# Optimization experiments

Hardware: AMD Instinct MI355X
Metric: run time of the kernel (lower is better)

The kernel has to match this reference:

```python
import jax, jax.numpy as jnp
import numpy as np

SEQ = 2048
HID = 1024
NH = 16
HD = HID // NH


def setup_inputs() -> dict:
    key = jax.random.key(0)
    ks = jax.random.split(key, 5)
    s = 0.02
    return {
        "hidden_states": jax.random.normal(ks[0], (SEQ, HID), dtype=jnp.float32),
        "w_attn": jax.random.normal(ks[1], (HID, 3 * HID), dtype=jnp.float32) * s,
        "b_attn": jax.random.normal(ks[2], (3 * HID,), dtype=jnp.float32) * s,
        "w_proj": jax.random.normal(ks[3], (HID, HID), dtype=jnp.float32) * s,
        "b_proj": jax.random.normal(ks[4], (HID,), dtype=jnp.float32) * s,
    }


def reference(hidden_states, w_attn, b_attn, w_proj, b_proj):
    S = hidden_states.shape[0]
    qkv = hidden_states @ w_attn + b_attn          # [S, 3H]
    q, k, v = jnp.split(qkv, 3, axis=-1)
    q = q.reshape(S, NH, HD)
    k = k.reshape(S, NH, HD)
    v = v.reshape(S, NH, HD)
    sm_scale = 1.0 / np.sqrt(HD).astype(np.float32)
    # explicit scores [h, q, k] in fp32, as in the torch module
    scores = jnp.einsum('qhd,khd->hqk', q.astype(jnp.float32), k.astype(jnp.float32))
    scores = scores * sm_scale
    causal = jnp.tril(jnp.ones((S, S), dtype=bool))  # [q, k]
    scores = jnp.where(causal[None, :, :], scores, -jnp.inf)
    probs = jax.nn.softmax(scores, axis=-1)
    attn = jnp.einsum('hqk,khd->qhd', probs, v.astype(jnp.float32))  # [S, NH, HD]
    attn = attn.reshape(S, HID).astype(hidden_states.dtype)
    return attn @ w_proj + b_proj
```

## Files before the change

kernel.cpp:

```cpp
#include <hip/hip_runtime.h>
#include <cstdint>
#include <cstddef>

#define SEQ 2048
#define HID 1024
#define NHEAD 16
#define HDIM 64

typedef _Float16 f16;
typedef f16 half8 __attribute__((ext_vector_type(8)));
typedef f16 half4 __attribute__((ext_vector_type(4)));
typedef f16 half2_ __attribute__((ext_vector_type(2)));
typedef float f32x4 __attribute__((ext_vector_type(4)));

#define ASYNC_COPY16(g, l)                                                    \
  __builtin_amdgcn_global_load_lds(                                           \
      (const __attribute__((address_space(1))) void*)(const void*)(g),        \
      (__attribute__((address_space(3))) void*)(void*)(l), 16, 0, 0)

__global__ __launch_bounds__(256) void prologue(
    const float* __restrict__ h, const float* __restrict__ wa,
    const float* __restrict__ wp, f16* __restrict__ h16,
    f16* __restrict__ waT, f16* __restrict__ wpT) {
  const int b = blockIdx.x, tid = threadIdx.x;
  if (b >= 1024) {
    int i = ((b - 1024) * 256 + tid) * 8;
    float4 v0 = *(const float4*)(h + i);
    float4 v1 = *(const float4*)(h + i + 4);
    half8 o;
    o[0] = (f16)v0.x; o[1] = (f16)v0.y; o[2] = (f16)v0.z; o[3] = (f16)v0.w;
    o[4] = (f16)v1.x; o[5] = (f16)v1.y; o[6] = (f16)v1.z; o[7] = (f16)v1.w;
    *(half8*)(h16 + i) = o;
    return;
  }
  const float* src; f16* dst; int C, bx, by;
  if (b < 768) { src = wa; dst = waT; C = 3072; bx = b % 48; by = b / 48; }
  else { int t = b - 768; src = wp; dst = wpT; C = 1024; bx = t & 15; by = t >> 4; }
  __shared__ float tile[64][65];
  const int tx = tid & 63, ty = tid >> 6;
  const int c0 = bx * 64, r0 = by * 64;
#pragma unroll
  for (int i = 0; i < 64; i += 4)
    tile[ty + i][tx] = src[(size_t)(r0 + ty + i) * C + c0 + tx];
  __syncthreads();
#pragma unroll
  for (int i = 0; i < 64; i += 4)
    dst[(size_t)(c0 + ty + i) * 1024 + r0 + tx] = (f16)tile[tx][ty + i];
}

template <int BM, int BN, bool OUT16>
__global__ __launch_bounds__(256) void gemm_f16(
    const f16* __restrict__ A, const f16* __restrict__ Bt,
    const float* __restrict__ bias, void* __restrict__ Cout, int M, int N,
    int K) {
  constexpr int FM = BM / 32, FN = BN / 32;
  __shared__ __align__(16) f16 sA[BM * 64];
  __shared__ __align__(16) f16 sB[BN * 64];
  const int tid = threadIdx.x;
  const int wave = tid >> 6, lane = tid & 63;
  const int quad = lane >> 4, l16 = lane & 15;
  const int m0 = blockIdx.y * BM, n0 = blockIdx.x * BN;
  const int wm = (wave >> 1) * (BM / 2), wn = (wave & 1) * (BN / 2);
  const int rowA = lane >> 3;
  const int chunkA = (lane & 7) ^ rowA;
  const int r7 = l16 & 7;

  f32x4 acc[FM][FN] = {};

  for (int k0 = 0; k0 < K; k0 += 64) {
#pragma unroll
    for (int r = wave; r < BM / 8; r += 4)
      ASYNC_COPY16(A + (size_t)(m0 + r * 8 + rowA) * K + k0 + chunkA * 8,
                   &sA[r * 512]);
#pragma unroll
    for (int r = wave; r < BN / 8; r += 4)
      ASYNC_COPY16(Bt + (size_t)(n0 + r * 8 + rowA) * K + k0 + chunkA * 8,
                   &sB[r * 512]);
    __syncthreads();

#pragma unroll
    for (int h = 0; h < 2; h++) {
      half8 af[FM], bf[FN];
#pragma unroll
      for (int i = 0; i < FM; i++)
        af[i] = *(const half8*)&sA[(wm + i * 16 + l16) * 64 +
                                   (((h << 2) | quad) ^ r7) * 8];
#pragma unroll
      for (int j = 0; j < FN; j++)
        bf[j] = *(const half8*)&sB[(wn + j * 16 + l16) * 64 +
                                   (((h << 2) | quad) ^ r7) * 8];
#pragma unroll
      for (int i = 0; i < FM; i++)
#pragma unroll
        for (int j = 0; j < FN; j++)
          acc[i][j] = __builtin_amdgcn_mfma_f32_16x16x32_f16(
              af[i], bf[j], acc[i][j], 0, 0, 0);
    }
    __syncthreads();
  }

#pragma unroll
  for (int i = 0; i < FM; i++) {
    int row = m0 + wm + i * 16 + quad * 4;
#pragma unroll
    for (int j = 0; j < FN; j++) {
      int col = n0 + wn + j * 16 + l16;
      float bv = bias[col];
#pragma unroll
      for (int r = 0; r < 4; r++) {
        float v = acc[i][j][r] + bv;
        if (OUT16)
          ((f16*)Cout)[(size_t)(row + r) * N + col] = (f16)v;
        else
          ((float*)Cout)[(size_t)(row + r) * N + col] = v;
      }
    }
  }
}

#define LROW 72
__global__ __launch_bounds__(256, 3) void attn_split(
    const f16* __restrict__ qkv, f16* __restrict__ out,
    f16* __restrict__ Opart, float* __restrict__ ml) {
  const int b = (blockIdx.x & 7) * 80 + (blockIdx.x >> 3);
  const int h = b / 40;
  const int t = b % 40;
  int m, c, nc;
  if (t < 4)       { m = t;                 c = 0;      nc = 1; }
  else if (t < 12) { int u = t - 4;  m = 4 + (u >> 1);  c = u & 1; nc = 2; }
  else if (t < 24) { int u = t - 12; m = 8 + u / 3;     c = u % 3; nc = 3; }
  else             { int u = t - 24; m = 12 + (u >> 2); c = u & 3; nc = 4; }
  const int q0 = m * 128;
  const int T = 2 * m + 2;
  const int kt0 = c * 8;
  const int kt1 = (kt0 + 8 < T) ? kt0 + 8 : T;
  const int maskFrom = 2 * m;

  __shared__ __align__(16) f16 sK[64 * LROW];
  __shared__ __align__(16) f16 sVt[64 * LROW];
  __shared__ __align__(16) f16 sP[4][32 * LROW];

  const int tid = threadIdx.x;
  const int wave = tid >> 6, lane = tid & 63;
  const int quad = lane >> 4, l16 = lane & 15;

  const f16 qs = (f16)0.18033688f;
  half8 qf[2][2];
#pragma unroll
  for (int g = 0; g < 2; g++) {
    const f16* qb = qkv + (size_t)(q0 + wave * 32 + g * 16 + l16) * 3072 +
                    h * HDIM + quad * 8;
    qf[g][0] = *(const half8*)qb;
    qf[g][1] = *(const half8*)(qb + 32);
#pragma unroll
    for (int j = 0; j < 8; j++) { qf[g][0][j] *= qs; qf[g][1][j] *= qs; }
  }

  const f16* kbase = qkv + HID + h * HDIM;
  const f16* vbase = qkv + 2 * HID + h * HDIM;
  const int ks_row = tid >> 3, ks_cc = tid & 7;
  const int vs_d = tid & 63, vs_g = tid >> 6;

  f32x4 o[2][4] = {};
  float m_i[2] = {-1e30f, -1e30f}, l_i[2] = {0.f, 0.f};
  half8 kreg[2], vreg[2];

  auto prefetch = [&](int kt) {
    const int k0 = kt * 64;
#pragma unroll
    for (int i = 0; i < 2; i++) {
      kreg[i] = *(const half8*)(kbase + (size_t)(k0 + ks_row + i * 32) * 3072 +
                                ks_cc * 8);
      half8 col;
#pragma unroll
      for (int j = 0; j < 8; j++)
        col[j] = vbase[(size_t)(k0 + (vs_g + i * 4) * 8 + j) * 3072 + vs_d];
      vreg[i] = col;
    }
  };

  prefetch(kt0);
  for (int kt = kt0; kt < kt1; kt++) {
    const int k0 = kt * 64;
#pragma unroll
    for (int i = 0; i < 2; i++) {
      *(half8*)&sK[(ks_row + i * 32) * LROW + ks_cc * 8] = kreg[i];
      *(half8*)&sVt[vs_d * LROW + (vs_g + i * 4) * 8] = vreg[i];
    }
    __syncthreads();
    if (kt + 1 < kt1) prefetch(kt + 1);

    f32x4 sacc[2][4] = {};
#pragma unroll
    for (int kb = 0; kb < 4; kb++) {
      half8 kf0 = *(const half8*)&sK[(kb * 16 + l16) * LROW + quad * 8];
      half8 kf1 = *(const half8*)&sK[(kb * 16 + l16) * LROW + 32 + quad * 8];
#pragma unroll
      for (int g = 0; g < 2; g++) {
        sacc[g][kb] = __builtin_amdgcn_mfma_f32_16x16x32_f16(kf0, qf[g][0],
                                                             sacc[g][kb], 0, 0, 0);
        sacc[g][kb] = __builtin_amdgcn_mfma_f32_16x16x32_f16(kf1, qf[g][1],
                                                             sacc[g][kb], 0, 0, 0);
      }
    }
    if (kt >= maskFrom) {
#pragma unroll
      for (int g = 0; g < 2; g++) {
        const int qg = q0 + wave * 32 + g * 16 + l16;
#pragma unroll
        for (int kb = 0; kb < 4; kb++) {
          int kg = k0 + kb * 16 + quad * 4;
#pragma unroll
          for (int r = 0; r < 4; r++)
            if (kg + r > qg) sacc[g][kb][r] = -1e30f;
        }
      }
    }
#pragma unroll
    for (int g = 0; g < 2; g++) {
      float mx = -1e30f;
#pragma unroll
      for (int kb = 0; kb < 4; kb++)
#pragma unroll
        for (int r = 0; r < 4; r++) mx = fmaxf(mx, sacc[g][kb][r]);
      mx = fmaxf(mx, __shfl_xor(mx, 16));
      mx = fmaxf(mx, __shfl_xor(mx, 32));
      if (!__all(mx <= m_i[g] + 8.f)) {
        const float mnew = fmaxf(m_i[g], mx);
        const float alpha = exp2f(m_i[g] - mnew);
        l_i[g] *= alpha;
#pragma unroll
        for (int j = 0; j < 4; j++)
#pragma unroll
          for (int r = 0; r < 4; r++) o[g][j][r] *= alpha;
        m_i[g] = mnew;
      }
      float rs = 0.f;
#pragma unroll
      for (int kb = 0; kb < 4; kb++)
#pragma unroll
        for (int r = 0; r < 4; r++) {
          float p = exp2f(sacc[g][kb][r] - m_i[g]);
          sacc[g][kb][r] = p;
          rs += p;
        }
      rs += __shfl_xor(rs, 16);
      rs += __shfl_xor(rs, 32);
      l_i[g] += rs;
      f16* pw = &sP[wave][(g * 16 + l16) * LROW];
#pragma unroll
      for (int kb = 0; kb < 4; kb++)
#pragma unroll
        for (int rp = 0; rp < 2; rp++) {
          half2_ pv;
          pv[0] = (f16)sacc[g][kb][rp * 2];
          pv[1] = (f16)sacc[g][kb][rp * 2 + 1];
          *(half2_*)&pw[kb * 16 + quad * 4 + rp * 2] = pv;
        }
    }
    half8 pf[2][2];
#pragma unroll
    for (int g = 0; g < 2; g++) {
      pf[g][0] = *(const half8*)&sP[wave][(g * 16 + l16) * LROW + quad * 8];
      pf[g][1] = *(const half8*)&sP[wave][(g * 16 + l16) * LROW + 32 + quad * 8];
    }
#pragma unroll
    for (int j = 0; j < 4; j++) {
      half8 vf0 = *(const half8*)&sVt[(j * 16 + l16) * LROW + quad * 8];
      half8 vf1 = *(const half8*)&sVt[(j * 16 + l16) * LROW + 32 + quad * 8];
#pragma unroll
      for (int g = 0; g < 2; g++) {
        o[g][j] = __builtin_amdgcn_mfma_f32_16x16x32_f16(vf0, pf[g][0], o[g][j], 0, 0, 0);
        o[g][j] = __builtin_amdgcn_mfma_f32_16x16x32_f16(vf1, pf[g][1], o[g][j], 0, 0, 0);
      }
    }
    __syncthreads();
  }

  if (nc == 1) {
#pragma unroll
    for (int g = 0; g < 2; g++) {
      const float inv = 1.f / l_i[g];
      f16* orow =
          out + (size_t)(q0 + wave * 32 + g * 16 + l16) * HID + h * HDIM;
#pragma unroll
      for (int j = 0; j < 4; j++) {
        half4 hv;
#pragma unroll
        for (int r = 0; r < 4; r++) hv[r] = (f16)(o[g][j][r] * inv);
        *(half4*)&orow[j * 16 + quad * 4] = hv;
      }
    }
  } else {
    int base;
    if (m < 8)       base = (m - 4) * 2;
    else if (m < 12) base = 8 + (m - 8) * 3;
    else             base = 20 + (m - 12) * 4;
    const int slot = h * 36 + base + c;
#pragma unroll
    for (int g = 0; g < 2; g++) {
      const int qrow = wave * 32 + g * 16 + l16;
      f16* op = Opart + (size_t)slot * 8192 + qrow * 64;
#pragma unroll
      for (int j = 0; j < 4; j++) {
        half4 hv;
#pragma unroll
        for (int r = 0; r < 4; r++) hv[r] = (f16)o[g][j][r];
        *(half4*)&op[j * 16 + quad * 4] = hv;
      }
      if (quad == 0) {
        ml[slot * 256 + qrow] = m_i[g];
        ml[slot * 256 + 128 + qrow] = l_i[g];
      }
    }
  }
}

__global__ __launch_bounds__(256) void attn_combine(
    const f16* __restrict__ Opart, const float* __restrict__ ml,
    f16* __restrict__ out) {
  int idx = blockIdx.x * 256 + threadIdx.x;
  int d4 = (idx & 15) * 4;
  int row = (idx >> 4) & 127;
  int rest = idx >> 11;
  int mi = rest % 12;
  int h = rest / 12;
  int m = 4 + mi;
  int nc = (mi < 4) ? 2 : (mi < 8) ? 3 : 4;
  int base = (mi < 4) ? mi * 2 : (mi < 8) ? 8 + (mi - 4) * 3 : 20 + (mi - 8) * 4;
  int slot0 = h * 36 + base;

  float mm[4], ll[4];
  float M = -1e30f;
#pragma unroll
  for (int cc = 0; cc < 4; cc++)
    if (cc < nc) {
      mm[cc] = ml[(slot0 + cc) * 256 + row];
      ll[cc] = ml[(slot0 + cc) * 256 + 128 + row];
      M = fmaxf(M, mm[cc]);
    }
  float L = 0.f, acc[4] = {0.f, 0.f, 0.f, 0.f};
#pragma unroll
  for (int cc = 0; cc < 4; cc++)
    if (cc < nc) {
      float w = exp2f(mm[cc] - M);
      L += w * ll[cc];
      half4 ov = *(const half4*)&Opart[(size_t)(slot0 + cc) * 8192 +
                                       row * 64 + d4];
#pragma unroll
      for (int r = 0; r < 4; r++) acc[r] += w * (float)ov[r];
    }
  const float invL = 1.f / L;
  half4 hv;
#pragma unroll
  for (int r = 0; r < 4; r++) hv[r] = (f16)(acc[r] * invL);
  *(half4*)&out[(size_t)(m * 128 + row) * HID + h * HDIM + d4] = hv;
}

extern "C" void kernel_launch(void* const* d_in, const int* in_sizes, int n_in,
                              void* d_out, int out_size, void* d_ws,
                              size_t ws_size, hipStream_t stream) {
  const float* h = (const float*)d_in[0];
  const float* wa = (const float*)d_in[1];
  const float* ba = (const float*)d_in[2];
  const float* wp = (const float*)d_in[3];
  const float* bp = (const float*)d_in[4];
  float* out = (float*)d_out;

  char* ws = (char*)d_ws;
  f16* h16 = (f16*)(ws);
  f16* waT = (f16*)(ws + (4u << 20));
  f16* wpT = (f16*)(ws + (10u << 20));
  f16* qkv = (f16*)(ws + (12u << 20));
  f16* attn = (f16*)(ws + (24u << 20));
  f16* Opart = (f16*)(ws);
  float* mlbuf = (float*)(ws + 9437184);

  prologue<<<2048, 256, 0, stream>>>(h, wa, wp, h16, waT, wpT);
  gemm_f16<64, 128, true><<<dim3(24, 32), 256, 0, stream>>>(
      h16, waT, ba, qkv, SEQ, 3 * HID, HID);
  attn_split<<<640, 256, 0, stream>>>(qkv, attn, Opart, mlbuf);
  attn_combine<<<1536, 256, 0, stream>>>(Opart, mlbuf, attn);
  gemm_f16<64, 64, false><<<dim3(16, 32), 256, 0, stream>>>(
      attn, wpT, bp, out, SEQ, HID, HID);
}
```

Baseline: 145.6 us.

## Double-buffer GEMM LDS tiles and widen P stores to half4

Doubles the shared-memory tiles in the f16 GEMM so the async global-to-LDS copy of the next K tile is issued before the MFMAs on the current tile, aiming to hide load latency. Separately, attention probability stores to LDS are merged from two half2 writes into one half4 write per block. The double buffering doubles GEMM LDS use, which may reduce occupancy. The visible loop shows no wait or barrier between the prefetch and the next iteration's reads, so correctness relies on the trailing __syncthreads (not shown) also waiting for the async copies.

```diff
diff --git a/kernel.cpp b/kernel.cpp
--- a/kernel.cpp
+++ b/kernel.cpp
@@ -54,8 +54,8 @@
     const float* __restrict__ bias, void* __restrict__ Cout, int M, int N,
     int K) {
   constexpr int FM = BM / 32, FN = BN / 32;
-  __shared__ __align__(16) f16 sA[BM * 64];
-  __shared__ __align__(16) f16 sB[BN * 64];
+  __shared__ __align__(16) f16 sA[2][BM * 64];
+  __shared__ __align__(16) f16 sB[2][BN * 64];
   const int tid = threadIdx.x;
   const int wave = tid >> 6, lane = tid & 63;
   const int quad = lane >> 4, l16 = lane & 15;
@@ -65,30 +65,37 @@
   const int chunkA = (lane & 7) ^ rowA;
   const int r7 = l16 & 7;
 
-  f32x4 acc[FM][FN] = {};
-
-  for (int k0 = 0; k0 < K; k0 += 64) {
+  auto stage = [&](int buf, int k0) {
 #pragma unroll
     for (int r = wave; r < BM / 8; r += 4)
       ASYNC_COPY16(A + (size_t)(m0 + r * 8 + rowA) * K + k0 + chunkA * 8,
-                   &sA[r * 512]);
+                   &sA[buf][r * 512]);
 #pragma unroll
     for (int r = wave; r < BN / 8; r += 4)
       ASYNC_COPY16(Bt + (size_t)(n0 + r * 8 + rowA) * K + k0 + chunkA * 8,
-                   &sB[r * 512]);
-    __syncthreads();
+                   &sB[buf][r * 512]);
+  };
+
+  f32x4 acc[FM][FN] = {};
+
+  stage(0, 0);
+  __syncthreads();
+  const int NT = K / 64;
+  for (int t = 0; t < NT; ++t) {
+    const int cur = t & 1;
+    if (t + 1 < NT) stage(cur ^ 1, (t + 1) * 64);
 
 #pragma unroll
     for (int h = 0; h < 2; h++) {
       half8 af[FM], bf[FN];
 #pragma unroll
       for (int i = 0; i < FM; i++)
-        af[i] = *(const half8*)&sA[(wm + i * 16 + l16) * 64 +
-                                   (((h << 2) | quad) ^ r7) * 8];
+        af[i] = *(const half8*)&sA[cur][(wm + i * 16 + l16) * 64 +
+                                        (((h << 2) | quad) ^ r7) * 8];
 #pragma unroll
       for (int j = 0; j < FN; j++)
-        bf[j] = *(const half8*)&sB[(wn + j * 16 + l16) * 64 +
-                                   (((h << 2) | quad) ^ r7) * 8];
+        bf[j] = *(const half8*)&sB[cur][(wn + j * 16 + l16) * 64 +
+                                        (((h << 2) | quad) ^ r7) * 8];
 #pragma unroll
       for (int i = 0; i < FM; i++)
 #pragma unroll
@@ -249,14 +256,12 @@
       l_i[g] += rs;
       f16* pw = &sP[wave][(g * 16 + l16) * LROW];
 #pragma unroll
-      for (int kb = 0; kb < 4; kb++)
-#pragma unroll
-        for (int rp = 0; rp < 2; rp++) {
-          half2_ pv;
-          pv[0] = (f16)sacc[g][kb][rp * 2];
-          pv[1] = (f16)sacc[g][kb][rp * 2 + 1];
-          *(half2_*)&pw[kb * 16 + quad * 4 + rp * 2] = pv;
-        }
+      for (int kb = 0; kb < 4; kb++) {
+        half4 pv;
+#pragma unroll
+        for (int r = 0; r < 4; r++) pv[r] = (f16)sacc[g][kb][r];
+        *(half4*)&pw[kb * 16 + quad * 4] = pv;
+      }
     }
     half8 pf[2][2];
 #pragma unroll
```

Measured after the change: 145.4 us. About the same (-0.1%).
